# Kernel tuning notes

Measured on AMD Instinct MI355X. Metric: run time of the kernel, lower is better.

## Reference

```python
import jax, jax.numpy as jnp
import numpy as np

NUM_HEADS = 8
EPS = 1e-5


def setup_inputs() -> dict:
    key = jax.random.key(0)
    ks = jax.random.split(key, 6)
    B, C, H, W = 8, 256, 32, 32
    s = 1.0 / np.sqrt(C)  # fan-in scale for 1x1 conv weights
    return {
        "x": jax.random.normal(ks[0], (B, C, H, W), jnp.float32),
        "Wq": jax.random.normal(ks[1], (C, C), jnp.float32) * s,
        "bq": jnp.zeros((C,), jnp.float32),
        "Wk": jax.random.normal(ks[2], (C, C), jnp.float32) * s,
        "bk": jnp.zeros((C,), jnp.float32),
        "Wv": jax.random.normal(ks[3], (C, C), jnp.float32) * s,
        "bv": jnp.zeros((C,), jnp.float32),
        "Wp": jax.random.normal(ks[4], (C, C), jnp.float32) * s,
        "bp": jnp.zeros((C,), jnp.float32),
        "gamma": jnp.ones((C,), jnp.float32),
        "beta": jnp.zeros((C,), jnp.float32),
    }


def _conv1x1(x, W, b):
    # 1x1 Conv2d == channel-mixing matmul: [B,C,H,W] -> [B,C,H,W]
    return jnp.einsum('oi,bihw->bohw', W, x) + b[None, :, None, None]


def reference(x, Wq, bq, Wk, bk, Wv, bv, Wp, bp, gamma, beta):
    B, C, H, W = x.shape
    nh = NUM_HEADS
    hd = C // nh
    HW = H * W

    q = _conv1x1(x, Wq, bq).reshape(B, nh, hd, HW)
    k = _conv1x1(x, Wk, bk).reshape(B, nh, hd, HW)
    v = _conv1x1(x, Wv, bv).reshape(B, nh, hd, HW)

    scores = jnp.einsum('bhdi,bhdj->bhij', q, k) / (hd ** 0.5)  # [B,nh,HW,HW]
    attn = jax.nn.softmax(scores, axis=-1)
    out = jnp.einsum('bhij,bhdj->bhdi', attn, v).reshape(B, C, H, W)

    out = _conv1x1(out, Wp, bp) + x  # residual

    # LayerNorm over channel dim (channels-last, as in original)
    o = out.transpose(0, 2, 3, 1)  # [B,H,W,C]
    mu = jnp.mean(o, axis=-1, keepdims=True)
    var = jnp.var(o, axis=-1, keepdims=True)
    o = (o - mu) * jax.lax.rsqrt(var + EPS) * gamma + beta
    return o.transpose(0, 3, 1, 2)
```

## Files before the change

### kernel.cpp

```cpp
#include <hip/hip_runtime.h>
#include <math.h>

#define NB 8
#define NC 256
#define NHW 1024
#define NHEADS 8
#define HD 32

typedef _Float16 half_t;
typedef __attribute__((ext_vector_type(8))) _Float16 half8;
typedef __attribute__((ext_vector_type(4))) _Float16 half4v;
typedef __attribute__((ext_vector_type(2))) _Float16 half2v;
typedef __attribute__((ext_vector_type(4))) float floatx4;

__device__ __forceinline__ half2v pk2(float a, float b) {
    union {
        __fp16 __attribute__((ext_vector_type(2))) r;
        half2v h;
    } u;
    u.r = __builtin_amdgcn_cvt_pkrtz(a, b);
    return u.h;
}
__device__ __forceinline__ void st8h(half_t* p, half2v a, half2v b) {
    union { half2v h[2]; uint2 u; } t;
    t.h[0] = a; t.h[1] = b;
    *(uint2*)p = t.u;
}
__device__ __forceinline__ half8 ldw8(const float* p) {
    float4 w0 = *(const float4*)p;
    float4 w1 = *(const float4*)(p + 4);
    union { half2v h2[4]; half8 h8; } u;
    u.h2[0] = pk2(w0.x, w0.y); u.h2[1] = pk2(w0.z, w0.w);
    u.h2[2] = pk2(w1.x, w1.y); u.h2[3] = pk2(w1.z, w1.w);
    return u.h8;
}

__global__ __launch_bounds__(256) void qkv_mfma(
    const float* __restrict__ x,
    const float* __restrict__ Wq, const float* __restrict__ Wk, const float* __restrict__ Wv,
    const float* __restrict__ bq, const float* __restrict__ bk, const float* __restrict__ bv,
    half_t* __restrict__ Qt, half_t* __restrict__ Kt, half_t* __restrict__ Vv)
{
    __shared__ half_t xs[64][264];

    int bz = blockIdx.z;
    int b = bz & 7, p = bz >> 3;
    const float* W    = (p == 0) ? Wq : (p == 1) ? Wk : Wv;
    const float* bias = (p == 0) ? bq : (p == 1) ? bk : bv;

    int t = threadIdx.x;
    int s0 = blockIdx.x * 64;
    const float* xb = x + (size_t)b * NC * NHW;

    {
        int sf = t & 15, cp = t >> 4;
        #pragma unroll
        for (int pass = 0; pass < 8; pass++) {
            int c = cp * 2 + 32 * pass;
            float4 a  = *(const float4*)&xb[(size_t)c * NHW + s0 + sf * 4];
            float4 bb = *(const float4*)&xb[(size_t)(c + 1) * NHW + s0 + sf * 4];
            *(half2v*)&xs[sf * 4 + 0][c] = pk2(a.x, bb.x);
            *(half2v*)&xs[sf * 4 + 1][c] = pk2(a.y, bb.y);
            *(half2v*)&xs[sf * 4 + 2][c] = pk2(a.z, bb.z);
            *(half2v*)&xs[sf * 4 + 3][c] = pk2(a.w, bb.w);
        }
    }
    __syncthreads();

    int wv = t >> 6, lane = t & 63;
    int mm = lane & 15, q = lane >> 4;
    int o0 = blockIdx.y * 128 + wv * 32;

    floatx4 acc[2][4];
    #pragma unroll
    for (int mt = 0; mt < 2; mt++)
        #pragma unroll
        for (int nt = 0; nt < 4; nt++) acc[mt][nt] = (floatx4){0.f, 0.f, 0.f, 0.f};

    #pragma unroll
    for (int k0 = 0; k0 < NC; k0 += 32) {
        half8 af[2], bf[4];
        #pragma unroll
        for (int mt = 0; mt < 2; mt++)
            af[mt] = ldw8(&W[(size_t)(o0 + mt * 16 + mm) * NC + k0 + q * 8]);
        #pragma unroll
        for (int nt = 0; nt < 4; nt++)
            bf[nt] = *(const half8*)&xs[nt * 16 + mm][k0 + q * 8];
        #pragma unroll
        for (int mt = 0; mt < 2; mt++)
            #pragma unroll
            for (int nt = 0; nt < 4; nt++)
                acc[mt][nt] = __builtin_amdgcn_mfma_f32_16x16x32_f16(af[mt], bf[nt], acc[mt][nt], 0, 0, 0);
    }

    int h  = (o0 >> 5);
    int bh = b * NHEADS + h;
    const float qs = 0.17677669529663687f * 1.4426950408889634f;

    #pragma unroll
    for (int mt = 0; mt < 2; mt++) {
        int d0 = mt * 16 + q * 4;
        float bb[4];
        #pragma unroll
        for (int r = 0; r < 4; r++) bb[r] = bias[o0 + mt * 16 + q * 4 + r];
        #pragma unroll
        for (int nt = 0; nt < 4; nt++) {
            int s = s0 + nt * 16 + mm;
            float v0 = acc[mt][nt][0] + bb[0], v1 = acc[mt][nt][1] + bb[1];
            float v2 = acc[mt][nt][2] + bb[2], v3 = acc[mt][nt][3] + bb[3];
            if (p == 0) { v0 *= qs; v1 *= qs; v2 *= qs; v3 *= qs; }
            if (p < 2) {
                half_t* out = (p == 0 ? Qt : Kt) + ((size_t)bh * NHW + s) * HD + d0;
                st8h(out, pk2(v0, v1), pk2(v2, v3));
            } else {
                Vv[((size_t)bh * HD + d0 + 0) * NHW + s] = (half_t)v0;
                Vv[((size_t)bh * HD + d0 + 1) * NHW + s] = (half_t)v1;
                Vv[((size_t)bh * HD + d0 + 2) * NHW + s] = (half_t)v2;
                Vv[((size_t)bh * HD + d0 + 3) * NHW + s] = (half_t)v3;
            }
        }
    }
}

__global__ __launch_bounds__(256) void attn_mfma(
    const half_t* __restrict__ Qt, const half_t* __restrict__ Kt,
    const half_t* __restrict__ Vv, half_t* __restrict__ At)
{
    __shared__ half_t Pl[4][2][2][16][36];
    __shared__ float Oz[4][32][34];
    __shared__ float Dz[4][32];

    int wv = threadIdx.x >> 6, lane = threadIdx.x & 63;
    int mm = lane & 15, q = lane >> 4;
    int L = blockIdx.x;
    int bh = L & 63, iblk = L >> 6;
    int b = bh >> 3, h = bh & 7;
    int i0 = iblk * 32;

    const half_t* Qb = Qt + (size_t)bh * NHW * HD;
    const half_t* Kb = Kt + (size_t)bh * NHW * HD;
    const half_t* Vb = Vv + (size_t)bh * HD * NHW;

    half8 qf0 = *(const half8*)&Qb[(size_t)(i0 + mm) * HD + q * 8];
    half8 qf1 = *(const half8*)&Qb[(size_t)(i0 + 16 + mm) * HD + q * 8];

    const int jb = wv * 256;
    floatx4 zero = (floatx4){0.f, 0.f, 0.f, 0.f};
    floatx4 oa00 = zero, oa01 = zero, oa10 = zero, oa11 = zero;
    float d0 = 0.f, d1 = 0.f;
    const _Float16 z = (_Float16)0.f;
    half8 pf_p0 = {z, z, z, z, z, z, z, z}, pf_p1 = pf_p0;

    half8 kc0 = *(const half8*)&Kb[(size_t)(jb + mm) * HD + q * 8];
    half8 kc1 = *(const half8*)&Kb[(size_t)(jb + 16 + mm) * HD + q * 8];
    half8 kn0 = *(const half8*)&Kb[(size_t)(jb + 32 + mm) * HD + q * 8];
    half8 kn1 = *(const half8*)&Kb[(size_t)(jb + 48 + mm) * HD + q * 8];
    half8 vc0 = *(const half8*)&Vb[(size_t)mm * NHW + jb + q * 8];
    half8 vc1 = *(const half8*)&Vb[(size_t)(16 + mm) * NHW + jb + q * 8];
    half8 vp0 = vc0, vp1 = vc1;

    #pragma unroll
    for (int it = 0; it < 8; it++) {
        floatx4 s00 = __builtin_amdgcn_mfma_f32_16x16x32_f16(kc0, qf0, zero, 0, 0, 0);
        floatx4 s01 = __builtin_amdgcn_mfma_f32_16x16x32_f16(kc1, qf0, zero, 0, 0, 0);
        floatx4 s10 = __builtin_amdgcn_mfma_f32_16x16x32_f16(kc0, qf1, zero, 0, 0, 0);
        floatx4 s11 = __builtin_amdgcn_mfma_f32_16x16x32_f16(kc1, qf1, zero, 0, 0, 0);

        int jk = jb + ((it + 2) & 7) * 32;
        int jv = jb + ((it + 1) & 7) * 32;
        half8 kf0 = *(const half8*)&Kb[(size_t)(jk + mm) * HD + q * 8];
        half8 kf1 = *(const half8*)&Kb[(size_t)(jk + 16 + mm) * HD + q * 8];
        half8 vn0 = *(const half8*)&Vb[(size_t)mm * NHW + jv + q * 8];
        half8 vn1 = *(const half8*)&Vb[(size_t)(16 + mm) * NHW + jv + q * 8];

        oa00 = __builtin_amdgcn_mfma_f32_16x16x32_f16(vp0, pf_p0, oa00, 0, 0, 0);
        oa01 = __builtin_amdgcn_mfma_f32_16x16x32_f16(vp1, pf_p0, oa01, 0, 0, 0);
        oa10 = __builtin_amdgcn_mfma_f32_16x16x32_f16(vp0, pf_p1, oa10, 0, 0, 0);
        oa11 = __builtin_amdgcn_mfma_f32_16x16x32_f16(vp1, pf_p1, oa11, 0, 0, 0);

        int buf = it & 1;
        {
            float e0 = exp2f(s00[0]), e1 = exp2f(s00[1]);
            float e2 = exp2f(s00[2]), e3 = exp2f(s00[3]);
            float f0 = exp2f(s01[0]), f1 = exp2f(s01[1]);
            float f2 = exp2f(s01[2]), f3 = exp2f(s01[3]);
            d0 += ((e0 + e1) + (e2 + e3)) + ((f0 + f1) + (f2 + f3));
            half_t (*PB)[36] = Pl[wv][0][buf];
            st8h(&PB[mm][q * 4],      pk2(e0, e1), pk2(e2, e3));
            st8h(&PB[mm][16 + q * 4], pk2(f0, f1), pk2(f2, f3));
        }
        {
            float e0 = exp2f(s10[0]), e1 = exp2f(s10[1]);
            float e2 = exp2f(s10[2]), e3 = exp2f(s10[3]);
            float f0 = exp2f(s11[0]), f1 = exp2f(s11[1]);
            float f2 = exp2f(s11[2]), f3 = exp2f(s11[3]);
            d1 += ((e0 + e1) + (e2 + e3)) + ((f0 + f1) + (f2 + f3));
            half_t (*PB)[36] = Pl[wv][1][buf];
            st8h(&PB[mm][q * 4],      pk2(e0, e1), pk2(e2, e3));
            st8h(&PB[mm][16 + q * 4], pk2(f0, f1), pk2(f2, f3));
        }
        union { half4v h4[2]; half8 h8; } u0, u1;
        u0.h4[0] = *(half4v*)&Pl[wv][0][buf][mm][q * 8];
        u0.h4[1] = *(half4v*)&Pl[wv][0][buf][mm][q * 8 + 4];
        u1.h4[0] = *(half4v*)&Pl[wv][1][buf][mm][q * 8];
        u1.h4[1] = *(half4v*)&Pl[wv][1][buf][mm][q * 8 + 4];

        kc0 = kn0; kc1 = kn1; kn0 = kf0; kn1 = kf1;
        vp0 = vc0; vp1 = vc1; vc0 = vn0; vc1 = vn1;
        pf_p0 = u0.h8; pf_p1 = u1.h8;
    }
    oa00 = __builtin_amdgcn_mfma_f32_16x16x32_f16(vp0, pf_p0, oa00, 0, 0, 0);
    oa01 = __builtin_amdgcn_mfma_f32_16x16x32_f16(vp1, pf_p0, oa01, 0, 0, 0);
    oa10 = __builtin_amdgcn_mfma_f32_16x16x32_f16(vp0, pf_p1, oa10, 0, 0, 0);
    oa11 = __builtin_amdgcn_mfma_f32_16x16x32_f16(vp1, pf_p1, oa11, 0, 0, 0);

    d0 += __shfl_xor(d0, 16); d0 += __shfl_xor(d0, 32);
    d1 += __shfl_xor(d1, 16); d1 += __shfl_xor(d1, 32);

    #pragma unroll
    for (int r = 0; r < 4; r++) {
        Oz[wv][q * 4 + r][mm]           = oa00[r];
        Oz[wv][16 + q * 4 + r][mm]      = oa01[r];
        Oz[wv][q * 4 + r][16 + mm]      = oa10[r];
        Oz[wv][16 + q * 4 + r][16 + mm] = oa11[r];
    }
    if (q == 0) { Dz[wv][mm] = d0; Dz[wv][16 + mm] = d1; }
    __syncthreads();

    int t = threadIdx.x;
    int iloc = t >> 3, dg = t & 7;
    float den = (Dz[0][iloc] + Dz[1][iloc]) + (Dz[2][iloc] + Dz[3][iloc]);
    float rinv = 1.f / den;
    float v[4];
    #pragma unroll
    for (int r = 0; r < 4; r++) {
        int d = dg * 4 + r;
        v[r] = ((Oz[0][d][iloc] + Oz[1][d][iloc]) + (Oz[2][d][iloc] + Oz[3][d][iloc])) * rinv;
    }
    half_t* dst = At + ((size_t)b * NHW + i0 + iloc) * NC + h * HD + dg * 4;
    st8h(dst, pk2(v[0], v[1]), pk2(v[2], v[3]));
}

__global__ __launch_bounds__(512) void projln(
    const half_t* __restrict__ At, const float* __restrict__ Wp,
    const float* __restrict__ bp, const float* __restrict__ x,
    const float* __restrict__ gamma, const float* __restrict__ beta,
    float* __restrict__ outp)
{
    __shared__ float tile[16][273];
    __shared__ float xs[256][17];
    __shared__ float Pz[4][64][17];
    __shared__ float ps[32][16], ps2[32][16];
    __shared__ float mu_s[16], rs_s[16];

    int t = threadIdx.x, wv = t >> 6, lane = t & 63;
    int mm = lane & 15, q = lane >> 4;
    int oh = wv & 3, kh = wv >> 2;
    int o0 = oh * 64;
    int b = blockIdx.y, s0 = blockIdx.x * 16;
    const half_t* ab = At + (size_t)b * NHW * NC;

    {
        int sL = t & 15, cb = t >> 4;
        #pragma unroll
        for (int pass = 0; pass < 8; pass++) {
            int c = pass * 32 + cb;
            xs[c][sL] = x[((size_t)b * NC + c) * NHW + s0 + sL];
        }
    }

    floatx4 acc[4];
    #pragma unroll
    for (int mt = 0; mt < 4; mt++) acc[mt] = (floatx4){0.f, 0.f, 0.f, 0.f};

    int kbase = kh * 128;
    #pragma unroll
    for (int kk = 0; kk < 128; kk += 32) {
        int k0 = kbase + kk;
        half8 bf = *(const half8*)&ab[(size_t)(s0 + mm) * NC + k0 + q * 8];
        #pragma unroll
        for (int mt = 0; mt < 4; mt++) {
            half8 af = ldw8(&Wp[(size_t)(o0 + mt * 16 + mm) * NC + k0 + q * 8]);
            acc[mt] = __builtin_amdgcn_mfma_f32_16x16x32_f16(af, bf, acc[mt], 0, 0, 0);
        }
    }

    if (kh == 1) {
        #pragma unroll
        for (int mt = 0; mt < 4; mt++)
            #pragma unroll
            for (int r = 0; r < 4; r++)
                Pz[oh][mt * 16 + q * 4 + r][mm] = acc[mt][r];
    }
    __syncthreads();
    if (kh == 0) {
        #pragma unroll
        for (int mt = 0; mt < 4; mt++) {
            #pragma unroll
            for (int r = 0; r < 4; r++) {
                int ol = mt * 16 + q * 4 + r;
                int o = o0 + ol;
                tile[mm][o] = acc[mt][r] + Pz[oh][ol][mm] + bp[o] + xs[o][mm];
            }
        }
    }
    __syncthreads();

    int sL = t & 15, part = t >> 4;
    float sum = 0.f, sq = 0.f;
    #pragma unroll
    for (int cc = 0; cc < 8; cc++) {
        float v = tile[sL][part * 8 + cc];
        sum += v; sq += v * v;
    }
    ps[part][sL] = sum; ps2[part][sL] = sq;
    __syncthreads();
    if (t < 16) {
        float S = 0.f, S2 = 0.f;
        #pragma unroll
        for (int p2 = 0; p2 < 32; p2++) { S += ps[p2][t]; S2 += ps2[p2][t]; }
        float mu  = S * (1.f / NC);
        float var = S2 * (1.f / NC) - mu * mu;
        mu_s[t] = mu;
        rs_s[t] = rsqrtf(var + 1e-5f);
    }
    __syncthreads();
    float mu = mu_s[sL], rs = rs_s[sL];
    float* ob = outp + (size_t)b * NC * NHW;
    #pragma unroll
    for (int cc = 0; cc < 8; cc++) {
        int c = part * 8 + cc;
        ob[(size_t)c * NHW + s0 + sL] = (tile[sL][c] - mu) * rs * gamma[c] + beta[c];
    }
}

extern "C" void kernel_launch(void* const* d_in, const int* in_sizes, int n_in,
                              void* d_out, int out_size, void* d_ws, size_t ws_size,
                              hipStream_t stream)
{
    const float* x     = (const float*)d_in[0];
    const float* Wq    = (const float*)d_in[1];
    const float* bq    = (const float*)d_in[2];
    const float* Wk    = (const float*)d_in[3];
    const float* bk    = (const float*)d_in[4];
    const float* Wv    = (const float*)d_in[5];
    const float* bv    = (const float*)d_in[6];
    const float* Wp    = (const float*)d_in[7];
    const float* bp    = (const float*)d_in[8];
    const float* gamma = (const float*)d_in[9];
    const float* beta  = (const float*)d_in[10];
    float* out = (float*)d_out;

    char* w = (char*)d_ws;
    half_t* Qt = (half_t*)(w);
    half_t* Kt = (half_t*)(w + ((size_t)4  << 20));
    half_t* Vv = (half_t*)(w + ((size_t)8  << 20));
    half_t* At = (half_t*)(w + ((size_t)12 << 20));

    qkv_mfma<<<dim3(16, 2, 24), 256, 0, stream>>>(x, Wq, Wk, Wv, bq, bk, bv, Qt, Kt, Vv);
    attn_mfma<<<dim3(2048), 256, 0, stream>>>(Qt, Kt, Vv, At);
    projln<<<dim3(64, 8), 512, 0, stream>>>(At, Wp, bp, x, gamma, beta, out);
}
```

Baseline: 139.9 us.

## Pre-convert QKV weights to fp16 and swizzle x tile in LDS

A small new kernel converts Wq/Wk/Wv to fp16 once per call, folding the softmax scale into Wq, so the QKV GEMM reads half-width weights without per-load conversion. The bias is pre-scaled instead of scaling the outputs. The x staging tile in shared memory now uses an XOR swizzle on columns to cut bank conflicts on fragment reads. The cost is one extra kernel launch, and the fp16 weight buffer shares workspace with At, which is only written later.

```diff
diff --git a/kernel.cpp b/kernel.cpp
--- a/kernel.cpp
+++ b/kernel.cpp
@@ -35,9 +35,27 @@
     return u.h8;
 }
 
+__global__ __launch_bounds__(256) void wprep(
+    const float* __restrict__ Wq, const float* __restrict__ Wk,
+    const float* __restrict__ Wv, half_t* __restrict__ Wh)
+{
+    int t = blockIdx.x * 256 + threadIdx.x;
+    int e = t * 8;
+    int m = e >> 16, off = e & 65535;
+    const float* src = (m == 0) ? Wq : (m == 1) ? Wk : Wv;
+    float sc = (m == 0) ? 0.17677669529663687f * 1.4426950408889634f : 1.f;
+    float4 a = *(const float4*)(src + off);
+    float4 b = *(const float4*)(src + off + 4);
+    union { half2v h2[4]; half8 h8; } u;
+    u.h2[0] = pk2(a.x * sc, a.y * sc);
+    u.h2[1] = pk2(a.z * sc, a.w * sc);
+    u.h2[2] = pk2(b.x * sc, b.y * sc);
+    u.h2[3] = pk2(b.z * sc, b.w * sc);
+    *(half8*)&Wh[e] = u.h8;
+}
+
 __global__ __launch_bounds__(256) void qkv_mfma(
-    const float* __restrict__ x,
-    const float* __restrict__ Wq, const float* __restrict__ Wk, const float* __restrict__ Wv,
+    const float* __restrict__ x, const half_t* __restrict__ Wh,
     const float* __restrict__ bq, const float* __restrict__ bk, const float* __restrict__ bv,
     half_t* __restrict__ Qt, half_t* __restrict__ Kt, half_t* __restrict__ Vv)
 {
@@ -45,8 +63,8 @@
 
     int bz = blockIdx.z;
     int b = bz & 7, p = bz >> 3;
-    const float* W    = (p == 0) ? Wq : (p == 1) ? Wk : Wv;
-    const float* bias = (p == 0) ? bq : (p == 1) ? bk : bv;
+    const half_t* Wf    = Wh + (size_t)p * 65536;
+    const float*  bias  = (p == 0) ? bq : (p == 1) ? bk : bv;
 
     int t = threadIdx.x;
     int s0 = blockIdx.x * 64;
@@ -54,15 +72,17 @@
 
     {
         int sf = t & 15, cp = t >> 4;
+        int sw = (sf & 7) << 3;
         #pragma unroll
         for (int pass = 0; pass < 8; pass++) {
             int c = cp * 2 + 32 * pass;
+            int cw = c ^ sw;
             float4 a  = *(const float4*)&xb[(size_t)c * NHW + s0 + sf * 4];
             float4 bb = *(const float4*)&xb[(size_t)(c + 1) * NHW + s0 + sf * 4];
-            *(half2v*)&xs[sf * 4 + 0][c] = pk2(a.x, bb.x);
-            *(half2v*)&xs[sf * 4 + 1][c] = pk2(a.y, bb.y);
-            *(half2v*)&xs[sf * 4 + 2][c] = pk2(a.z, bb.z);
-            *(half2v*)&xs[sf * 4 + 3][c] = pk2(a.w, bb.w);
+            *(half2v*)&xs[sf * 4 + 0][cw] = pk2(a.x, bb.x);
+            *(half2v*)&xs[sf * 4 + 1][cw] = pk2(a.y, bb.y);
+            *(half2v*)&xs[sf * 4 + 2][cw] = pk2(a.z, bb.z);
+            *(half2v*)&xs[sf * 4 + 3][cw] = pk2(a.w, bb.w);
         }
     }
     __syncthreads();
@@ -82,10 +102,13 @@
         half8 af[2], bf[4];
         #pragma unroll
         for (int mt = 0; mt < 2; mt++)
-            af[mt] = ldw8(&W[(size_t)(o0 + mt * 16 + mm) * NC + k0 + q * 8]);
-        #pragma unroll
-        for (int nt = 0; nt < 4; nt++)
-            bf[nt] = *(const half8*)&xs[nt * 16 + mm][k0 + q * 8];
+            af[mt] = *(const half8*)&Wf[(size_t)(o0 + mt * 16 + mm) * NC + k0 + q * 8];
+        #pragma unroll
+        for (int nt = 0; nt < 4; nt++) {
+            int row = nt * 16 + mm;
+            int col = (k0 + q * 8) ^ (((row >> 2) & 7) << 3);
+            bf[nt] = *(const half8*)&xs[row][col];
+        }
         #pragma unroll
         for (int mt = 0; mt < 2; mt++)
             #pragma unroll
@@ -96,19 +119,19 @@
     int h  = (o0 >> 5);
     int bh = b * NHEADS + h;
     const float qs = 0.17677669529663687f * 1.4426950408889634f;
+    float bsc = (p == 0) ? qs : 1.f;
 
     #pragma unroll
     for (int mt = 0; mt < 2; mt++) {
         int d0 = mt * 16 + q * 4;
         float bb[4];
         #pragma unroll
-        for (int r = 0; r < 4; r++) bb[r] = bias[o0 + mt * 16 + q * 4 + r];
+        for (int r = 0; r < 4; r++) bb[r] = bias[o0 + mt * 16 + q * 4 + r] * bsc;
         #pragma unroll
         for (int nt = 0; nt < 4; nt++) {
             int s = s0 + nt * 16 + mm;
             float v0 = acc[mt][nt][0] + bb[0], v1 = acc[mt][nt][1] + bb[1];
             float v2 = acc[mt][nt][2] + bb[2], v3 = acc[mt][nt][3] + bb[3];
-            if (p == 0) { v0 *= qs; v1 *= qs; v2 *= qs; v3 *= qs; }
             if (p < 2) {
                 half_t* out = (p == 0 ? Qt : Kt) + ((size_t)bh * NHW + s) * HD + d0;
                 st8h(out, pk2(v0, v1), pk2(v2, v3));
@@ -356,8 +379,10 @@
     half_t* Kt = (half_t*)(w + ((size_t)4  << 20));
     half_t* Vv = (half_t*)(w + ((size_t)8  << 20));
     half_t* At = (half_t*)(w + ((size_t)12 << 20));
-
-    qkv_mfma<<<dim3(16, 2, 24), 256, 0, stream>>>(x, Wq, Wk, Wv, bq, bk, bv, Qt, Kt, Vv);
+    half_t* Wh = (half_t*)(w + ((size_t)12 << 20));
+
+    wprep<<<dim3(96), 256, 0, stream>>>(Wq, Wk, Wv, Wh);
+    qkv_mfma<<<dim3(16, 2, 24), 256, 0, stream>>>(x, Wh, bq, bk, bv, Qt, Kt, Vv);
     attn_mfma<<<dim3(2048), 256, 0, stream>>>(Qt, Kt, Vv, At);
     projln<<<dim3(64, 8), 512, 0, stream>>>(At, Wp, bp, x, gamma, beta, out);
 }
```

Result: faster. 136.7 us (-2.3%).
